# Kernel optimization log

Hardware: AMD Instinct MI355X
Metric: run time of the kernel (lower is better)

Reference implementation:

```python
import jax, jax.numpy as jnp
import numpy as np


def setup_inputs() -> dict:
    key = jax.random.key(0)
    k1, k2, k3 = jax.random.split(key, 3)
    N, E, D_IN, D_OUT = 100000, 1600000, 64, 64
    x = jax.random.normal(k1, (N, D_IN), dtype=jnp.float32)
    edge_index = jax.random.randint(k2, (2, E), 0, N, dtype=jnp.int64)
    # Glorot-style init for the GCN weight, zero bias (PyG defaults)
    W = jax.random.normal(k3, (D_IN, D_OUT), dtype=jnp.float32) * (1.0 / np.sqrt(D_IN))
    b = jnp.zeros((D_OUT,), dtype=jnp.float32)
    return {"x": x, "edge_index": edge_index, "W": W, "b": b}


def reference(x, edge_index, W, b):
    # GCNConv (PyG semantics, add_self_loops=True, normalize=True) followed by
    # Dropout (eval mode -> identity) and ReLU.
    N = x.shape[0]
    # Linear transform first (small GEMM)
    xw = x @ W  # [N, D_OUT]
    # Add self-loops
    loops = jnp.arange(N, dtype=edge_index.dtype)
    row = jnp.concatenate([edge_index[0], loops])  # source nodes
    col = jnp.concatenate([edge_index[1], loops])  # destination nodes
    # Symmetric degree normalization: deg over destination index (PyG gcn_norm)
    ones = jnp.ones(col.shape[0], dtype=xw.dtype)
    deg = jax.ops.segment_sum(ones, col, num_segments=N)
    deg_inv_sqrt = jnp.where(deg > 0, jax.lax.rsqrt(deg), 0.0)
    norm = deg_inv_sqrt[row] * deg_inv_sqrt[col]  # [E+N]
    # Gather source features, scale, scatter-add to destinations
    msgs = norm[:, None] * xw[row]  # [E+N, D_OUT]
    out = jax.ops.segment_sum(msgs, col, num_segments=N)
    out = out + b
    # dropout in eval mode is identity
    return jax.nn.relu(out)
```

## Files before the change

### kernel.cpp

```cpp
#include <hip/hip_runtime.h>
#include <hip/hip_fp16.h>


#define D 64
#define BW 256
#define CAP 6144
#define PART_T 256
#define EPB 4096
#define SCAN_CHUNK 1024

typedef __attribute__((ext_vector_type(8))) short bf16x8;
typedef __attribute__((ext_vector_type(4))) float f32x4;

__device__ __forceinline__ unsigned short f2bf(float f) {
    unsigned u = __float_as_uint(f);
    u += 0x7FFFu + ((u >> 16) & 1u);
    return (unsigned short)(u >> 16);
}

__global__ __launch_bounds__(256, 4)
void k_gemm(const float* __restrict__ x, const float* __restrict__ W,
            unsigned short* __restrict__ xw_h, int N) {
    __shared__ float Ws[64 * 64];
    int tid = threadIdx.x;
    for (int i = tid; i < 4096; i += 256) Ws[i] = W[i];
    __syncthreads();
    int lane = tid & 63, wv = tid >> 6;
    int m = lane & 15, quad = lane >> 4;
    bf16x8 Bf[4][2];
#pragma unroll
    for (int t = 0; t < 4; ++t)
#pragma unroll
        for (int s = 0; s < 2; ++s) {
            bf16x8 f;
#pragma unroll
            for (int j = 0; j < 8; ++j)
                f[j] = (short)f2bf(Ws[(s * 32 + quad * 8 + j) * 64 + t * 16 + m]);
            Bf[t][s] = f;
        }
    int row0 = (blockIdx.x * 4 + wv) * 16;
    if (row0 >= N) return;
    const float* xr = x + (size_t)(row0 + m) * 64 + quad * 8;
    float4 a0 = *(const float4*)(xr);
    float4 a1 = *(const float4*)(xr + 4);
    float4 a2 = *(const float4*)(xr + 32);
    float4 a3 = *(const float4*)(xr + 36);
    bf16x8 A0, A1;
    A0[0] = (short)f2bf(a0.x); A0[1] = (short)f2bf(a0.y);
    A0[2] = (short)f2bf(a0.z); A0[3] = (short)f2bf(a0.w);
    A0[4] = (short)f2bf(a1.x); A0[5] = (short)f2bf(a1.y);
    A0[6] = (short)f2bf(a1.z); A0[7] = (short)f2bf(a1.w);
    A1[0] = (short)f2bf(a2.x); A1[1] = (short)f2bf(a2.y);
    A1[2] = (short)f2bf(a2.z); A1[3] = (short)f2bf(a2.w);
    A1[4] = (short)f2bf(a3.x); A1[5] = (short)f2bf(a3.y);
    A1[6] = (short)f2bf(a3.z); A1[7] = (short)f2bf(a3.w);
    f32x4 acc[4];
#pragma unroll
    for (int t = 0; t < 4; ++t) {
        acc[t] = (f32x4){0.f, 0.f, 0.f, 0.f};
        acc[t] = __builtin_amdgcn_mfma_f32_16x16x32_bf16(A0, Bf[t][0], acc[t], 0, 0, 0);
        acc[t] = __builtin_amdgcn_mfma_f32_16x16x32_bf16(A1, Bf[t][1], acc[t], 0, 0, 0);
    }
#pragma unroll
    for (int t = 0; t < 4; ++t)
#pragma unroll
        for (int r = 0; r < 4; ++r)
            xw_h[(size_t)(row0 + quad * 4 + r) * 64 + t * 16 + m] =
                __half_as_ushort(__float2half(acc[t][r]));
}

__global__ void k_hist1(const int* __restrict__ col, int* __restrict__ hist,
                        int E, int NB1, int NBUCK) {
    extern __shared__ int lhist[];
    int bk = blockIdx.x;
    for (int bu = threadIdx.x; bu < NBUCK; bu += PART_T) lhist[bu] = 0;
    __syncthreads();
    int base = bk * EPB;
#pragma unroll 4
    for (int i = threadIdx.x; i < EPB; i += PART_T) {
        int e = base + i;
        if (e < E) atomicAdd(&lhist[col[e] >> 8], 1);
    }
    __syncthreads();
    for (int bu = threadIdx.x; bu < NBUCK; bu += PART_T)
        hist[bu * NB1 + bk] = lhist[bu];
}

__global__ void k_blocksum(const int* __restrict__ src, int* __restrict__ partial, int L) {
    int base = blockIdx.x * SCAN_CHUNK;
    int s = 0;
    for (int i = threadIdx.x; i < SCAN_CHUNK; i += 256) {
        int idx = base + i;
        s += (idx < L) ? src[idx] : 0;
    }
#pragma unroll
    for (int off = 32; off > 0; off >>= 1) s += __shfl_down(s, off);
    __shared__ int ws[4];
    if ((threadIdx.x & 63) == 0) ws[threadIdx.x >> 6] = s;
    __syncthreads();
    if (threadIdx.x == 0) partial[blockIdx.x] = ws[0] + ws[1] + ws[2] + ws[3];
}

__global__ void k_scan_partials(int* __restrict__ partial, int P) {
    __shared__ int wtot[4];
    int i = threadIdx.x;
    int v = (i < P) ? partial[i] : 0;
    int lane = i & 63, wv = i >> 6;
    int s = v;
#pragma unroll
    for (int off = 1; off < 64; off <<= 1) {
        int t = __shfl_up(s, off);
        if (lane >= off) s += t;
    }
    if (lane == 63) wtot[wv] = s;
    __syncthreads();
    int woff = 0;
    for (int w = 0; w < 4; ++w) woff += (w < wv) ? wtot[w] : 0;
    if (i < P) partial[i] = woff + s - v;
}

__global__ void k_scan_excl(const int* __restrict__ src, const int* __restrict__ partial,
                            int* __restrict__ dst, int L) {
    __shared__ int wsum[4];
    int lane = threadIdx.x & 63, wv = threadIdx.x >> 6;
    int base = blockIdx.x * SCAN_CHUNK + threadIdx.x * 4;
    int v0 = (base + 0 < L) ? src[base + 0] : 0;
    int v1 = (base + 1 < L) ? src[base + 1] : 0;
    int v2 = (base + 2 < L) ? src[base + 2] : 0;
    int v3 = (base + 3 < L) ? src[base + 3] : 0;
    int t = v0 + v1 + v2 + v3;
    int s = t;
#pragma unroll
    for (int off = 1; off < 64; off <<= 1) {
        int u = __shfl_up(s, off);
        if (lane >= off) s += u;
    }
    if (lane == 63) wsum[wv] = s;
    __syncthreads();
    int woff = 0;
    for (int w = 0; w < 4; ++w) woff += (w < wv) ? wsum[w] : 0;
    int excl = partial[blockIdx.x] + woff + (s - t);
    if (base + 0 < L) dst[base + 0] = excl;
    if (base + 1 < L) dst[base + 1] = excl + v0;
    if (base + 2 < L) dst[base + 2] = excl + v0 + v1;
    if (base + 3 < L) dst[base + 3] = excl + v0 + v1 + v2;
}

__global__ void k_scatter1(const int* __restrict__ row, const int* __restrict__ col,
                           const int* __restrict__ histS, int* __restrict__ packed,
                           int E, int NB1, int NBUCK) {
    extern __shared__ int cur[];
    int bk = blockIdx.x;
    for (int bu = threadIdx.x; bu < NBUCK; bu += PART_T)
        cur[bu] = histS[bu * NB1 + bk];
    __syncthreads();
    int base = bk * EPB;
#pragma unroll 4
    for (int i = threadIdx.x; i < EPB; i += PART_T) {
        int e = base + i;
        if (e < E) {
            int c = col[e], r = row[e];
            int pos = atomicAdd(&cur[c >> 8], 1);
            packed[pos] = (r << 8) | (c & 255);
        }
    }
}

__global__ void k_dis(const int* __restrict__ histS, const int* __restrict__ packed,
                      float* __restrict__ disg, int E, int NB1, int NBUCK, int N) {
    __shared__ int lh[BW];
    int b = blockIdx.x;
    int lo = histS[b * NB1];
    int hi = (b == NBUCK - 1) ? E : histS[(b + 1) * NB1];
    lh[threadIdx.x] = 0;
    __syncthreads();
    for (int i = lo + threadIdx.x; i < hi; i += BW)
        atomicAdd(&lh[packed[i] & 255], 1);
    __syncthreads();
    int n = b * BW + threadIdx.x;
    if (n < N) disg[n] = rsqrtf((float)(lh[threadIdx.x] + 1));
}

__global__ __launch_bounds__(1024, 8)
void k_gather(const int* __restrict__ histS, const int* __restrict__ packed,
              const float* __restrict__ disg, const uint2* __restrict__ xwh,
              const float* __restrict__ bias, float4* __restrict__ out4,
              int E, int NB1, int NBUCK, int N) {
    __shared__ int lh[BW], stt[BW], cur[BW];
    __shared__ int srtL[CAP];
    __shared__ int wsum[4];
    int b = blockIdx.x;
    int tid = threadIdx.x;
    if (tid < BW) lh[tid] = 0;
    __syncthreads();
    int lo = histS[b * NB1];
    int hi = (b == NBUCK - 1) ? E : histS[(b + 1) * NB1];
    int sz = min(hi - lo, CAP);
    const int* pk = packed + lo;
    for (int i = tid; i < sz; i += 1024)
        atomicAdd(&lh[pk[i] & 255], 1);
    __syncthreads();
    int lane = tid & 63, wv4 = tid >> 6;
    int v = (tid < BW) ? lh[tid] : 0;
    int s = v;
#pragma unroll
    for (int off = 1; off < 64; off <<= 1) {
        int u = __shfl_up(s, off);
        if (lane >= off) s += u;
    }
    if (tid < BW && lane == 63) wsum[wv4] = s;
    __syncthreads();
    if (tid < BW) {
        int woff = 0;
        for (int w = 0; w < 4; ++w) woff += (w < wv4) ? wsum[w] : 0;
        int st = woff + s - v;
        stt[tid] = st;
        cur[tid] = st;
    }
    __syncthreads();
    for (int i = tid; i < sz; i += 1024) {
        int p = pk[i];
        int pos = atomicAdd(&cur[p & 255], 1);
        srtL[pos] = p >> 8;
    }
    __syncthreads();
    int wv = tid >> 6;
    int q = lane >> 4;
    int l = lane & 15;
    const float4 bb = ((const float4*)bias)[l];
#define ADDS(h, ww)                                                         \
    {                                                                       \
        __half2 h0 = *(__half2*)&(h).x, h1 = *(__half2*)&(h).y;             \
        float2 f0 = __half22float2(h0), f1 = __half22float2(h1);            \
        acc.x = fmaf((ww), f0.x, acc.x); acc.y = fmaf((ww), f0.y, acc.y);   \
        acc.z = fmaf((ww), f1.x, acc.z); acc.w = fmaf((ww), f1.y, acc.w);   \
    }
    for (int nn = wv * 16; nn < wv * 16 + 16; ++nn) {
        int node = b * BW + nn;
        if (node >= N) break;
        int k = lh[nn], s0 = stt[nn];
        float dn = rsqrtf((float)(k + 1));
        float4 acc = make_float4(0.f, 0.f, 0.f, 0.f);
        if (q == 0) {
            uint2 hs = xwh[(size_t)node * 16 + l];
            ADDS(hs, dn);
        }
        int j = q;
        for (; j + 12 < k; j += 16) {
            int r0 = srtL[s0 + j];
            int r1 = srtL[s0 + j + 4];
            int r2 = srtL[s0 + j + 8];
            int r3 = srtL[s0 + j + 12];
            float w0 = disg[r0], w1 = disg[r1], w2 = disg[r2], w3 = disg[r3];
            uint2 va = xwh[(size_t)r0 * 16 + l];
            uint2 vb = xwh[(size_t)r1 * 16 + l];
            uint2 vc = xwh[(size_t)r2 * 16 + l];
            uint2 vd = xwh[(size_t)r3 * 16 + l];
            ADDS(va, w0); ADDS(vb, w1); ADDS(vc, w2); ADDS(vd, w3);
        }
        for (; j < k; j += 4) {
            int r = srtL[s0 + j];
            float wr = disg[r];
            uint2 ve = xwh[(size_t)r * 16 + l];
            ADDS(ve, wr);
        }
#pragma unroll
        for (int mm = 16; mm < 64; mm <<= 1) {
            acc.x += __shfl_xor(acc.x, mm);
            acc.y += __shfl_xor(acc.y, mm);
            acc.z += __shfl_xor(acc.z, mm);
            acc.w += __shfl_xor(acc.w, mm);
        }
        if (q == 0) {
            float4 o;
            o.x = fmaxf(fmaf(dn, acc.x, bb.x), 0.f);
            o.y = fmaxf(fmaf(dn, acc.y, bb.y), 0.f);
            o.z = fmaxf(fmaf(dn, acc.z, bb.z), 0.f);
            o.w = fmaxf(fmaf(dn, acc.w, bb.w), 0.f);
            out4[(size_t)node * 16 + l] = o;
        }
    }
#undef ADDS
}

extern "C" void kernel_launch(void* const* d_in, const int* in_sizes, int n_in,
                              void* d_out, int out_size, void* d_ws, size_t ws_size,
                              hipStream_t stream) {
    const float* x    = (const float*)d_in[0];
    const int*   ei   = (const int*)d_in[1];
    const float* W    = (const float*)d_in[2];
    const float* bias = (const float*)d_in[3];
    float* out = (float*)d_out;

    const int N = in_sizes[0] / D;
    const int E = in_sizes[1] / 2;
    const int* row = ei;
    const int* col = ei + E;

    const int NBUCK = (N + BW - 1) / BW;
    const int NB1   = (E + EPB - 1) / EPB;
    const int L     = NBUCK * NB1;
    const int P     = (L + SCAN_CHUNK - 1) / SCAN_CHUNK;
    const int NT    = (N + 15) / 16;

    char* ws = (char*)d_ws;
    size_t off = 0;
    unsigned short* xw_h = (unsigned short*)(ws + off);
    off += (size_t)N * D * sizeof(unsigned short);
    int*   packed  = (int*)(ws + off);   off += (size_t)E * sizeof(int);
    int*   hist    = (int*)(ws + off);   off += (size_t)L * sizeof(int);
    int*   histS   = (int*)(ws + off);   off += (size_t)L * sizeof(int);
    float* disg    = (float*)(ws + off); off += (size_t)N * sizeof(float);
    int*   partial = (int*)(ws + off);   off += 256 * sizeof(int);

    size_t lds1 = (size_t)NBUCK * sizeof(int);

    k_gemm<<<(NT + 3) / 4, 256, 0, stream>>>(x, W, xw_h, N);
    k_hist1<<<NB1, PART_T, lds1, stream>>>(col, hist, E, NB1, NBUCK);
    k_blocksum<<<P, 256, 0, stream>>>(hist, partial, L);
    k_scan_partials<<<1, 256, 0, stream>>>(partial, P);
    k_scan_excl<<<P, 256, 0, stream>>>(hist, partial, histS, L);
    k_scatter1<<<NB1, PART_T, lds1, stream>>>(row, col, histS, packed, E, NB1, NBUCK);
    k_dis<<<NBUCK, BW, 0, stream>>>(histS, packed, disg, E, NB1, NBUCK, N);
    k_gather<<<NBUCK, 1024, 0, stream>>>(histS, packed, disg, (const uint2*)xw_h,
                                         bias, (float4*)out, E, NB1, NBUCK, N);
}
```

Baseline: 175.4 us.

## Fuse histogram into GEMM launch and fold bucket scan into scatter

The edge-bucket histogram now runs as extra blocks of the GEMM kernel. The three-kernel global scan is replaced by having each scatter block compute its own per-bucket prefix and bucket totals directly from the histogram, which cuts the launch count from eight to four. Bucket width drops from 256 to 128 nodes, the gather block shrinks to 512 threads, and edges per partition block double. The cost is that every scatter block redundantly reads the whole histogram, about NB1×NBUCK loads per block, which may make that kernel latency-bound.

```diff
diff --git a/kernel.cpp b/kernel.cpp
--- a/kernel.cpp
+++ b/kernel.cpp
@@ -3,11 +3,10 @@
 
 
 #define D 64
-#define BW 256
-#define CAP 6144
-#define PART_T 256
-#define EPB 4096
-#define SCAN_CHUNK 1024
+#define BW 128
+#define CAP 3072
+#define EPB 8192
+#define MAXBUCK 800
 
 typedef __attribute__((ext_vector_type(8))) short bf16x8;
 typedef __attribute__((ext_vector_type(4))) float f32x4;
@@ -19,10 +18,28 @@
 }
 
 __global__ __launch_bounds__(256, 4)
-void k_gemm(const float* __restrict__ x, const float* __restrict__ W,
-            unsigned short* __restrict__ xw_h, int N) {
-    __shared__ float Ws[64 * 64];
+void k_gemm_hist(const float* __restrict__ x, const float* __restrict__ W,
+                 unsigned short* __restrict__ xw_h, const int* __restrict__ col,
+                 int* __restrict__ hist, int E, int N, int NB1, int NBUCK) {
+    __shared__ float sh[4096];
     int tid = threadIdx.x;
+    if ((int)blockIdx.x < NB1) {
+        int* lh = (int*)sh;
+        int bk = blockIdx.x;
+        for (int bu = tid; bu < NBUCK; bu += 256) lh[bu] = 0;
+        __syncthreads();
+        int base = bk * EPB;
+#pragma unroll 4
+        for (int i = tid; i < EPB; i += 256) {
+            int e = base + i;
+            if (e < E) atomicAdd(&lh[col[e] >> 7], 1);
+        }
+        __syncthreads();
+        for (int bu = tid; bu < NBUCK; bu += 256)
+            hist[bk * NBUCK + bu] = lh[bu];
+        return;
+    }
+    float* Ws = sh;
     for (int i = tid; i < 4096; i += 256) Ws[i] = W[i];
     __syncthreads();
     int lane = tid & 63, wv = tid >> 6;
@@ -38,7 +55,7 @@
                 f[j] = (short)f2bf(Ws[(s * 32 + quad * 8 + j) * 64 + t * 16 + m]);
             Bf[t][s] = f;
         }
-    int row0 = (blockIdx.x * 4 + wv) * 16;
+    int row0 = ((blockIdx.x - NB1) * 4 + wv) * 16;
     if (row0 >= N) return;
     const float* xr = x + (size_t)(row0 + m) * 64 + quad * 8;
     float4 a0 = *(const float4*)(xr);
@@ -69,67 +86,33 @@
                 __half_as_ushort(__float2half(acc[t][r]));
 }
 
-__global__ void k_hist1(const int* __restrict__ col, int* __restrict__ hist,
-                        int E, int NB1, int NBUCK) {
-    extern __shared__ int lhist[];
-    int bk = blockIdx.x;
-    for (int bu = threadIdx.x; bu < NBUCK; bu += PART_T) lhist[bu] = 0;
-    __syncthreads();
-    int base = bk * EPB;
-#pragma unroll 4
-    for (int i = threadIdx.x; i < EPB; i += PART_T) {
-        int e = base + i;
-        if (e < E) atomicAdd(&lhist[col[e] >> 8], 1);
-    }
-    __syncthreads();
-    for (int bu = threadIdx.x; bu < NBUCK; bu += PART_T)
-        hist[bu * NB1 + bk] = lhist[bu];
-}
-
-__global__ void k_blocksum(const int* __restrict__ src, int* __restrict__ partial, int L) {
-    int base = blockIdx.x * SCAN_CHUNK;
-    int s = 0;
-    for (int i = threadIdx.x; i < SCAN_CHUNK; i += 256) {
-        int idx = base + i;
-        s += (idx < L) ? src[idx] : 0;
-    }
-#pragma unroll
-    for (int off = 32; off > 0; off >>= 1) s += __shfl_down(s, off);
-    __shared__ int ws[4];
-    if ((threadIdx.x & 63) == 0) ws[threadIdx.x >> 6] = s;
-    __syncthreads();
-    if (threadIdx.x == 0) partial[blockIdx.x] = ws[0] + ws[1] + ws[2] + ws[3];
-}
-
-__global__ void k_scan_partials(int* __restrict__ partial, int P) {
-    __shared__ int wtot[4];
-    int i = threadIdx.x;
-    int v = (i < P) ? partial[i] : 0;
-    int lane = i & 63, wv = i >> 6;
-    int s = v;
-#pragma unroll
-    for (int off = 1; off < 64; off <<= 1) {
-        int t = __shfl_up(s, off);
-        if (lane >= off) s += t;
-    }
-    if (lane == 63) wtot[wv] = s;
-    __syncthreads();
-    int woff = 0;
-    for (int w = 0; w < 4; ++w) woff += (w < wv) ? wtot[w] : 0;
-    if (i < P) partial[i] = woff + s - v;
-}
-
-__global__ void k_scan_excl(const int* __restrict__ src, const int* __restrict__ partial,
-                            int* __restrict__ dst, int L) {
+__global__ __launch_bounds__(256, 4)
+void k_scatter(const int* __restrict__ row, const int* __restrict__ col,
+               const int* __restrict__ hist, int* __restrict__ packed,
+               int* __restrict__ bstart, int E, int NB1, int NBUCK) {
+    __shared__ int pref[MAXBUCK];
+    __shared__ int cur[MAXBUCK];
     __shared__ int wsum[4];
-    int lane = threadIdx.x & 63, wv = threadIdx.x >> 6;
-    int base = blockIdx.x * SCAN_CHUNK + threadIdx.x * 4;
-    int v0 = (base + 0 < L) ? src[base + 0] : 0;
-    int v1 = (base + 1 < L) ? src[base + 1] : 0;
-    int v2 = (base + 2 < L) ? src[base + 2] : 0;
-    int v3 = (base + 3 < L) ? src[base + 3] : 0;
-    int t = v0 + v1 + v2 + v3;
-    int s = t;
+    int bk = blockIdx.x, tid = threadIdx.x;
+    for (int bu = tid; bu < NBUCK; bu += 256) {
+        int tot = 0, pf = 0;
+        for (int k = 0; k < NB1; ++k) {
+            int h = hist[k * NBUCK + bu];
+            tot += h;
+            pf += (k < bk) ? h : 0;
+        }
+        pref[bu] = pf;
+        cur[bu] = tot;
+    }
+    __syncthreads();
+    int i0 = tid * 4;
+    int v0 = (i0 + 0 < NBUCK) ? cur[i0 + 0] : 0;
+    int v1 = (i0 + 1 < NBUCK) ? cur[i0 + 1] : 0;
+    int v2 = (i0 + 2 < NBUCK) ? cur[i0 + 2] : 0;
+    int v3 = (i0 + 3 < NBUCK) ? cur[i0 + 3] : 0;
+    int t4 = v0 + v1 + v2 + v3;
+    int lane = tid & 63, wv = tid >> 6;
+    int s = t4;
 #pragma unroll
     for (int off = 1; off < 64; off <<= 1) {
         int u = __shfl_up(s, off);
@@ -139,68 +122,65 @@
     __syncthreads();
     int woff = 0;
     for (int w = 0; w < 4; ++w) woff += (w < wv) ? wsum[w] : 0;
-    int excl = partial[blockIdx.x] + woff + (s - t);
-    if (base + 0 < L) dst[base + 0] = excl;
-    if (base + 1 < L) dst[base + 1] = excl + v0;
-    if (base + 2 < L) dst[base + 2] = excl + v0 + v1;
-    if (base + 3 < L) dst[base + 3] = excl + v0 + v1 + v2;
-}
-
-__global__ void k_scatter1(const int* __restrict__ row, const int* __restrict__ col,
-                           const int* __restrict__ histS, int* __restrict__ packed,
-                           int E, int NB1, int NBUCK) {
-    extern __shared__ int cur[];
-    int bk = blockIdx.x;
-    for (int bu = threadIdx.x; bu < NBUCK; bu += PART_T)
-        cur[bu] = histS[bu * NB1 + bk];
+    int excl = woff + s - t4;
+    __syncthreads();
+    if (i0 + 0 < NBUCK) cur[i0 + 0] = excl + pref[i0 + 0];
+    if (i0 + 1 < NBUCK) cur[i0 + 1] = excl + v0 + pref[i0 + 1];
+    if (i0 + 2 < NBUCK) cur[i0 + 2] = excl + v0 + v1 + pref[i0 + 2];
+    if (i0 + 3 < NBUCK) cur[i0 + 3] = excl + v0 + v1 + v2 + pref[i0 + 3];
+    if (bk == 0) {
+        if (i0 + 0 < NBUCK) bstart[i0 + 0] = excl;
+        if (i0 + 1 < NBUCK) bstart[i0 + 1] = excl + v0;
+        if (i0 + 2 < NBUCK) bstart[i0 + 2] = excl + v0 + v1;
+        if (i0 + 3 < NBUCK) bstart[i0 + 3] = excl + v0 + v1 + v2;
+        if (tid == 0) bstart[NBUCK] = E;
+    }
     __syncthreads();
     int base = bk * EPB;
 #pragma unroll 4
-    for (int i = threadIdx.x; i < EPB; i += PART_T) {
+    for (int i = tid; i < EPB; i += 256) {
         int e = base + i;
         if (e < E) {
             int c = col[e], r = row[e];
-            int pos = atomicAdd(&cur[c >> 8], 1);
-            packed[pos] = (r << 8) | (c & 255);
-        }
-    }
-}
-
-__global__ void k_dis(const int* __restrict__ histS, const int* __restrict__ packed,
-                      float* __restrict__ disg, int E, int NB1, int NBUCK, int N) {
+            int pos = atomicAdd(&cur[c >> 7], 1);
+            packed[pos] = (r << 7) | (c & 127);
+        }
+    }
+}
+
+__global__ void k_dis(const int* __restrict__ bstart, const int* __restrict__ packed,
+                      float* __restrict__ disg, int N) {
     __shared__ int lh[BW];
-    int b = blockIdx.x;
-    int lo = histS[b * NB1];
-    int hi = (b == NBUCK - 1) ? E : histS[(b + 1) * NB1];
-    lh[threadIdx.x] = 0;
-    __syncthreads();
-    for (int i = lo + threadIdx.x; i < hi; i += BW)
-        atomicAdd(&lh[packed[i] & 255], 1);
-    __syncthreads();
-    int n = b * BW + threadIdx.x;
-    if (n < N) disg[n] = rsqrtf((float)(lh[threadIdx.x] + 1));
-}
-
-__global__ __launch_bounds__(1024, 8)
-void k_gather(const int* __restrict__ histS, const int* __restrict__ packed,
+    int b = blockIdx.x, tid = threadIdx.x;
+    if (tid < BW) lh[tid] = 0;
+    __syncthreads();
+    int lo = bstart[b], hi = bstart[b + 1];
+    for (int i = lo + tid; i < hi; i += 256)
+        atomicAdd(&lh[packed[i] & 127], 1);
+    __syncthreads();
+    if (tid < BW) {
+        int n = b * BW + tid;
+        if (n < N) disg[n] = rsqrtf((float)(lh[tid] + 1));
+    }
+}
+
+__global__ __launch_bounds__(512, 4)
+void k_gather(const int* __restrict__ bstart, const int* __restrict__ packed,
               const float* __restrict__ disg, const uint2* __restrict__ xwh,
-              const float* __restrict__ bias, float4* __restrict__ out4,
-              int E, int NB1, int NBUCK, int N) {
+              const float* __restrict__ bias, float4* __restrict__ out4, int N) {
     __shared__ int lh[BW], stt[BW], cur[BW];
     __shared__ int srtL[CAP];
-    __shared__ int wsum[4];
-    int b = blockIdx.x;
-    int tid = threadIdx.x;
+    __shared__ int wsum[2];
+    int b = blockIdx.x, tid = threadIdx.x;
     if (tid < BW) lh[tid] = 0;
     __syncthreads();
-    int lo = histS[b * NB1];
-    int hi = (b == NBUCK - 1) ? E : histS[(b + 1) * NB1];
+    int lo = bstart[b], hi = bstart[b + 1];
     int sz = min(hi - lo, CAP);
     const int* pk = packed + lo;
-    for (int i = tid; i < sz; i += 1024)
-        atomicAdd(&lh[pk[i] & 255], 1);
-    __syncthreads();
-    int lane = tid & 63, wv4 = tid >> 6;
+    for (int i = tid; i < sz; i += 512)
+        atomicAdd(&lh[pk[i] & 127], 1);
+    __syncthreads();
+    int lane = tid & 63, wv = tid >> 6;
     int v = (tid < BW) ? lh[tid] : 0;
     int s = v;
 #pragma unroll
@@ -208,23 +188,20 @@
         int u = __shfl_up(s, off);
         if (lane >= off) s += u;
     }
-    if (tid < BW && lane == 63) wsum[wv4] = s;
+    if (tid < BW && lane == 63) wsum[wv] = s;
     __syncthreads();
     if (tid < BW) {
-        int woff = 0;
-        for (int w = 0; w < 4; ++w) woff += (w < wv4) ? wsum[w] : 0;
-        int st = woff + s - v;
+        int st = ((wv == 1) ? wsum[0] : 0) + s - v;
         stt[tid] = st;
         cur[tid] = st;
     }
     __syncthreads();
-    for (int i = tid; i < sz; i += 1024) {
+    for (int i = tid; i < sz; i += 512) {
         int p = pk[i];
-        int pos = atomicAdd(&cur[p & 255], 1);
-        srtL[pos] = p >> 8;
-    }
-    __syncthreads();
-    int wv = tid >> 6;
+        int pos = atomicAdd(&cur[p & 127], 1);
+        srtL[pos] = p >> 7;
+    }
+    __syncthreads();
     int q = lane >> 4;
     int l = lane & 15;
     const float4 bb = ((const float4*)bias)[l];
@@ -299,29 +276,21 @@
 
     const int NBUCK = (N + BW - 1) / BW;
     const int NB1   = (E + EPB - 1) / EPB;
-    const int L     = NBUCK * NB1;
-    const int P     = (L + SCAN_CHUNK - 1) / SCAN_CHUNK;
     const int NT    = (N + 15) / 16;
+    const int GB    = (NT + 3) / 4;
 
     char* ws = (char*)d_ws;
     size_t off = 0;
     unsigned short* xw_h = (unsigned short*)(ws + off);
     off += (size_t)N * D * sizeof(unsigned short);
-    int*   packed  = (int*)(ws + off);   off += (size_t)E * sizeof(int);
-    int*   hist    = (int*)(ws + off);   off += (size_t)L * sizeof(int);
-    int*   histS   = (int*)(ws + off);   off += (size_t)L * sizeof(int);
-    float* disg    = (float*)(ws + off); off += (size_t)N * sizeof(float);
-    int*   partial = (int*)(ws + off);   off += 256 * sizeof(int);
-
-    size_t lds1 = (size_t)NBUCK * sizeof(int);
-
-    k_gemm<<<(NT + 3) / 4, 256, 0, stream>>>(x, W, xw_h, N);
-    k_hist1<<<NB1, PART_T, lds1, stream>>>(col, hist, E, NB1, NBUCK);
-    k_blocksum<<<P, 256, 0, stream>>>(hist, partial, L);
-    k_scan_partials<<<1, 256, 0, stream>>>(partial, P);
-    k_scan_excl<<<P, 256, 0, stream>>>(hist, partial, histS, L);
-    k_scatter1<<<NB1, PART_T, lds1, stream>>>(row, col, histS, packed, E, NB1, NBUCK);
-    k_dis<<<NBUCK, BW, 0, stream>>>(histS, packed, disg, E, NB1, NBUCK, N);
-    k_gather<<<NBUCK, 1024, 0, stream>>>(histS, packed, disg, (const uint2*)xw_h,
-                                         bias, (float4*)out, E, NB1, NBUCK, N);
-}
+    int*   packed = (int*)(ws + off);   off += (size_t)E * sizeof(int);
+    int*   hist   = (int*)(ws + off);   off += (size_t)NB1 * NBUCK * sizeof(int);
+    int*   bstart = (int*)(ws + off);   off += (size_t)(NBUCK + 1) * sizeof(int);
+    float* disg   = (float*)(ws + off); off += (size_t)N * sizeof(float);
+
+    k_gemm_hist<<<NB1 + GB, 256, 0, stream>>>(x, W, xw_h, col, hist, E, N, NB1, NBUCK);
+    k_scatter<<<NB1, 256, 0, stream>>>(row, col, hist, packed, bstart, E, NB1, NBUCK);
+    k_dis<<<NBUCK, 256, 0, stream>>>(bstart, packed, disg, N);
+    k_gather<<<NBUCK, 512, 0, stream>>>(bstart, packed, disg, (const uint2*)xw_h,
+                                        bias, (float4*)out, N);
+}
```

Measured after the change: 322.8 us. 84.0% more time.
